# Optimization experiments

Measured on AMD Instinct MI355X. Metric: run time of the kernel, lower is better.

## Reference

```python
import jax, jax.numpy as jnp
import numpy as np

H = 128; NC = 100000; ND = 20000; NG = 50000; E = 150000; EP = 100000; L = 2

def _ln(x, g, b, eps=1e-5):
    mu = jnp.mean(x, -1, keepdims=True)
    v = jnp.mean((x - mu) ** 2, -1, keepdims=True)
    return (x - mu) * jax.lax.rsqrt(v + eps) * g + b

def _gelu(x):
    return jax.nn.gelu(x, approximate=False)  # torch nn.GELU default = exact erf

def _sage(x_src, x_dst, ei, Wl, bl, Wr):
    # PyG SAGEConv: mean-aggregate src features over incoming edges, lin_l(agg)+bias + lin_r(x_dst)
    n_dst = x_dst.shape[0]
    msg = x_src[ei[0]]                                   # [E, H] gather
    s = jax.ops.segment_sum(msg, ei[1], num_segments=n_dst)
    cnt = jax.ops.segment_sum(jnp.ones((ei.shape[1],), x_src.dtype), ei[1], num_segments=n_dst)
    agg = s / jnp.maximum(cnt, 1.0)[:, None]             # zero for isolated dst nodes
    return agg @ Wl + bl + x_dst @ Wr

def _make_ei(k, ns, nd, e):
    k1, k2 = jax.random.split(k)
    return jnp.stack([jax.random.randint(k1, (e,), 0, ns, dtype=jnp.int32),
                      jax.random.randint(k2, (e,), 0, nd, dtype=jnp.int32)])

def setup_inputs() -> dict:
    key = jax.random.key(0)
    ks = jax.random.split(key, 16)
    s = 0.05
    return {
        "x_chem": jax.random.normal(ks[0], (NC, 128), jnp.float32),
        "x_dis": jax.random.normal(ks[1], (ND, 128), jnp.float32),
        "gene_emb": jax.random.normal(ks[2], (NG, H), jnp.float32) * s,
        "proj_W": jax.random.normal(ks[3], (2, 128, H), jnp.float32) * s,
        "proj_b": jnp.zeros((2, H), jnp.float32),
        "proj_ln_g": jnp.ones((2, H), jnp.float32),
        "proj_ln_b": jnp.zeros((2, H), jnp.float32),
        "sage_Wl": jax.random.normal(ks[4], (L, 4, H, H), jnp.float32) * s,
        "sage_bl": jnp.zeros((L, 4, H), jnp.float32),
        "sage_Wr": jax.random.normal(ks[5], (L, 4, H, H), jnp.float32) * s,
        "ln_g": jnp.ones((L, 3, H), jnp.float32),
        "ln_b": jnp.zeros((L, 3, H), jnp.float32),
        "W_cd": jax.random.normal(ks[6], (H, H), jnp.float32) * s,
        "ei_c2d": _make_ei(ks[7], NC, ND, E),
        "ei_d2c": _make_ei(ks[8], ND, NC, E),
        "ei_c2g": _make_ei(ks[9], NC, NG, E),
        "ei_g2c": _make_ei(ks[10], NG, NC, E),
        "pos_edge": _make_ei(ks[11], NC, ND, EP),
        "neg_edge": _make_ei(ks[12], NC, ND, EP),
    }

def reference(x_chem, x_dis, gene_emb, proj_W, proj_b, proj_ln_g, proj_ln_b,
              sage_Wl, sage_bl, sage_Wr, ln_g, ln_b, W_cd,
              ei_c2d, ei_d2c, ei_c2g, ei_g2c, pos_edge, neg_edge):
    # init node states: Linear+LN+GELU for featured ntypes, embedding table for gene
    hc = _gelu(_ln(x_chem @ proj_W[0] + proj_b[0], proj_ln_g[0], proj_ln_b[0]))
    hd = _gelu(_ln(x_dis @ proj_W[1] + proj_b[1], proj_ln_g[1], proj_ln_b[1]))
    hg = gene_emb
    for l in range(L):
        # HeteroConv aggr='mean': chemical receives d2c (idx1) and g2c (idx3) -> mean of 2
        nc = 0.5 * (_sage(hd, hc, ei_d2c, sage_Wl[l, 1], sage_bl[l, 1], sage_Wr[l, 1])
                    + _sage(hg, hc, ei_g2c, sage_Wl[l, 3], sage_bl[l, 3], sage_Wr[l, 3]))
        nd = _sage(hc, hd, ei_c2d, sage_Wl[l, 0], sage_bl[l, 0], sage_Wr[l, 0])
        ng = _sage(hc, hg, ei_c2g, sage_Wl[l, 2], sage_bl[l, 2], sage_Wr[l, 2])
        # residual + LN + GELU (dropout is identity in eval mode)
        hc = _gelu(_ln(nc + hc, ln_g[l, 0], ln_b[l, 0]))
        hd = _gelu(_ln(nd + hd, ln_g[l, 1], ln_b[l, 1]))
        hg = _gelu(_ln(ng + hg, ln_g[l, 2], ln_b[l, 2]))
    def dec(ei):
        return ((hc[ei[0]] @ W_cd) * hd[ei[1]]).sum(-1)
    return dec(pos_edge), dec(neg_edge)
```

## Files before the change

kernel.cpp:

```cpp
#include <hip/hip_runtime.h>

#define HD 128

constexpr int T_NC = 100000;
constexpr int T_ND = 20000;
constexpr int T_NG = 50000;
constexpr int T_E  = 150000;
constexpr int T_EP = 100000;
constexpr int NMAT = 21;
constexpr int DEGN = 2 * T_NC + T_ND + T_NG;

typedef __attribute__((ext_vector_type(8))) short   s16x8;
typedef __attribute__((ext_vector_type(8))) __bf16  bf16x8;
typedef __attribute__((ext_vector_type(4))) float   f32x4;

union Frag { s16x8 s; bf16x8 b; };

__device__ __forceinline__ float gelu_f(float x) {
    return 0.5f * x * (1.0f + erff(x * 0.70710678118654752f));
}

__global__ void pack_weights(const float* __restrict__ proj_W,
                             const float* __restrict__ sage_Wl,
                             const float* __restrict__ sage_Wr,
                             const float* __restrict__ W_cd,
                             unsigned short* __restrict__ phi,
                             unsigned short* __restrict__ plo)
{
    int m = blockIdx.x;
    const float* W;
    const float* W2 = nullptr;
    bool transp = false;
    if (m < 2)        W = proj_W  + (size_t)m * HD * HD;
    else if (m < 10)  W = sage_Wl + (size_t)(m - 2) * HD * HD;
    else if (m < 18)  W = sage_Wr + (size_t)(m - 10) * HD * HD;
    else if (m == 18) { W = W_cd; transp = true; }
    else {
        int l = m - 19;
        W  = sage_Wr + (size_t)(l * 4 + 1) * HD * HD;
        W2 = sage_Wr + (size_t)(l * 4 + 3) * HD * HD;
    }

    int t = threadIdx.x;
    int kstep = t >> 6;
    int lane  = t & 63;
    int kbase = kstep * 32 + (lane >> 4) * 8;
    int c     = lane & 15;
    for (int cb = 0; cb < 8; ++cb) {
        int col = cb * 16 + c;
        size_t off = ((((size_t)m * 8 + cb) * 4 + kstep) * 64 + lane) * 8;
        #pragma unroll
        for (int j = 0; j < 8; ++j) {
            int k = kbase + j;
            float w = transp ? W[(size_t)col * HD + k] : W[(size_t)k * HD + col];
            if (W2) w += W2[(size_t)k * HD + col];
            __bf16 h = (__bf16)w;
            union { __bf16 b; unsigned short u; } ch, cl;
            ch.b = h;
            cl.b = (__bf16)(w - (float)h);
            phi[off + j] = ch.u;
            plo[off + j] = cl.u;
        }
    }
}

__global__ void conv_gene(const float* __restrict__ src, unsigned short* __restrict__ dst)
{
    size_t i = (size_t)(blockIdx.x * blockDim.x + threadIdx.x) * 8;
    if (i >= (size_t)T_NG * HD) return;
    f32x4 a0 = *(const f32x4*)(src + i);
    f32x4 a1 = *(const f32x4*)(src + i + 4);
    Frag u;
    u.b[0] = (__bf16)a0.x; u.b[1] = (__bf16)a0.y; u.b[2] = (__bf16)a0.z; u.b[3] = (__bf16)a0.w;
    u.b[4] = (__bf16)a1.x; u.b[5] = (__bf16)a1.y; u.b[6] = (__bf16)a1.z; u.b[7] = (__bf16)a1.w;
    *(s16x8*)(dst + i) = u.s;
}

__global__ void edge_count4(const int* __restrict__ eA, const int* __restrict__ eB,
                            const int* __restrict__ eC, const int* __restrict__ eD,
                            int gPer, int* __restrict__ deg)
{
    int seg = blockIdx.x / gPer;
    int e = (blockIdx.x % gPer) * 256 + threadIdx.x;
    if (e >= T_E) return;
    const int* ei = seg == 0 ? eA : seg == 1 ? eB : seg == 2 ? eC : eD;
    int off = seg == 0 ? 0 : seg == 1 ? T_NC : seg == 2 ? 2 * T_NC : 2 * T_NC + T_ND;
    atomicAdd(&deg[off + ei[T_E + e]], 1);
}

__global__ void scan_local(const int* __restrict__ deg, int* __restrict__ rp,
                           int* __restrict__ bsum, int N)
{
    __shared__ int wtot[4];
    int t = threadIdx.x;
    int lane = t & 63, w = t >> 6;
    int base = blockIdx.x * 1024 + t * 4;
    int v[4];
    #pragma unroll
    for (int j = 0; j < 4; ++j) v[j] = (base + j < N) ? deg[base + j] : 0;
    int p1 = v[0] + v[1];
    int p2 = p1 + v[2];
    int total = p2 + v[3];
    int sc = total;
    #pragma unroll
    for (int o = 1; o < 64; o <<= 1) {
        int y = __shfl_up(sc, o);
        if (lane >= o) sc += y;
    }
    if (lane == 63) wtot[w] = sc;
    __syncthreads();
    int woff = 0;
    for (int i = 0; i < w; ++i) woff += wtot[i];
    int ex = woff + sc - total;
    if (base + 0 < N) rp[base + 0] = ex;
    if (base + 1 < N) rp[base + 1] = ex + v[0];
    if (base + 2 < N) rp[base + 2] = ex + p1;
    if (base + 3 < N) rp[base + 3] = ex + p2;
    if (t == 255) bsum[blockIdx.x] = woff + sc;
}

__global__ void scan_tops(int* __restrict__ bsum, int B)
{
    int lane = threadIdx.x;
    int off = 0;
    for (int s = 0; s < B; s += 64) {
        int i = s + lane;
        int v = (i < B) ? bsum[i] : 0;
        int sc = v;
        #pragma unroll
        for (int o = 1; o < 64; o <<= 1) {
            int y = __shfl_up(sc, o);
            if (lane >= o) sc += y;
        }
        if (i < B) bsum[i] = off + sc - v;
        off += __shfl(sc, 63);
    }
}

__global__ void scan_add(int* __restrict__ rp, const int* __restrict__ bsum, int N)
{
    int base = blockIdx.x * 1024 + threadIdx.x * 4;
    int o = bsum[blockIdx.x];
    #pragma unroll
    for (int j = 0; j < 4; ++j)
        if (base + j < N) rp[base + j] += o;
}

__global__ void edge_fill4(const int* __restrict__ eA, const int* __restrict__ eB,
                           const int* __restrict__ eC, const int* __restrict__ eD,
                           int gPer, const int* __restrict__ rp,
                           int* __restrict__ fil, int* __restrict__ col)
{
    int seg = blockIdx.x / gPer;
    int e = (blockIdx.x % gPer) * 256 + threadIdx.x;
    if (e >= T_E) return;
    const int* ei = seg == 0 ? eA : seg == 1 ? eB : seg == 2 ? eC : eD;
    int off = seg == 0 ? 0 : seg == 1 ? T_NC : seg == 2 ? 2 * T_NC : 2 * T_NC + T_ND;
    int d = ei[T_E + e];
    int p = rp[off + d] + atomicAdd(&fil[off + d], 1);
    col[p] = ei[e];
}

struct Pair {
    const void* A;
    const int* rp; const int* dg; const int* col;
    int w; int fmt;
};
struct Seg {
    Pair p0, p1, p2;
    const float *bias0, *bias1, *g_ln, *b_ln;
    unsigned short* out;
    float scale;
    int np, use_res, M, nblk;
};

template<int MODE>
__global__ __launch_bounds__(256, 8)
void fused_gemm(Seg s0, Seg s1, Seg s2,
                const unsigned short* __restrict__ phi,
                const unsigned short* __restrict__ plo)
{
    __shared__ __align__(16) unsigned short As_hi[32 * HD];
    __shared__ __align__(16) unsigned short As_lo[32 * HD];
    __shared__ float psum[4][32];
    __shared__ float psq[4][32];

    int bid = blockIdx.x;
    Seg s;
    if (bid < s0.nblk) s = s0;
    else if (bid < s0.nblk + s1.nblk) { bid -= s0.nblk; s = s1; }
    else { bid -= s0.nblk + s1.nblk; s = s2; }

    const int tid  = threadIdx.x;
    const int w    = tid >> 6;
    const int lane = tid & 63;
    const int c    = lane & 15;
    const int hi4  = lane >> 4;
    const int row0 = bid * 32;

    f32x4 acc[2][2];
    #pragma unroll
    for (int rb = 0; rb < 2; ++rb)
        #pragma unroll
        for (int q = 0; q < 2; ++q) acc[rb][q] = (f32x4)0.f;

    for (int p = 0; p < s.np; ++p) {
        Pair P = (p == 0) ? s.p0 : (p == 1) ? s.p1 : s.p2;
        const bool gath = (P.rp != nullptr);

        __syncthreads();
        for (int it = 0; it < 2; ++it) {
            int u  = tid + it * 256;
            int r  = u >> 4;
            int k8 = (u & 15) * 8;
            int gr = row0 + r;
            Frag vh, vl;
            vh.s = (s16x8)0; vl.s = (s16x8)0;
            if (gr < s.M) {
                if (gath) {
                    float av[8] = {0.f, 0.f, 0.f, 0.f, 0.f, 0.f, 0.f, 0.f};
                    int st = P.rp[gr];
                    int d  = P.dg[gr];
                    const unsigned short* Ah = (const unsigned short*)P.A;
                    int i = 0;
                    for (; i + 2 <= d; i += 2) {
                        int e0 = P.col[st + i];
                        int e1 = P.col[st + i + 1];
                        Frag x0, x1;
                        x0.s = *(const s16x8*)(Ah + (size_t)e0 * HD + k8);
                        x1.s = *(const s16x8*)(Ah + (size_t)e1 * HD + k8);
                        #pragma unroll
                        for (int j = 0; j < 8; ++j)
                            av[j] += (float)x0.b[j] + (float)x1.b[j];
                    }
                    if (i < d) {
                        int e0 = P.col[st + i];
                        Frag x0;
                        x0.s = *(const s16x8*)(Ah + (size_t)e0 * HD + k8);
                        #pragma unroll
                        for (int j = 0; j < 8; ++j)
                            av[j] += (float)x0.b[j];
                    }
                    float rs = 1.f / (float)(d > 1 ? d : 1);
                    #pragma unroll
                    for (int j = 0; j < 8; ++j) {
                        float x = av[j] * rs;
                        __bf16 h = (__bf16)x;
                        vh.b[j] = h;
                        vl.b[j] = (__bf16)(x - (float)h);
                    }
                } else if (P.fmt) {
                    vh.s = *(const s16x8*)((const unsigned short*)P.A + (size_t)gr * HD + k8);
                } else {
                    const f32x4* ap = (const f32x4*)((const float*)P.A + (size_t)gr * HD + k8);
                    f32x4 a0 = ap[0], a1 = ap[1];
                    vh.b[0] = (__bf16)a0.x; vh.b[1] = (__bf16)a0.y;
                    vh.b[2] = (__bf16)a0.z; vh.b[3] = (__bf16)a0.w;
                    vh.b[4] = (__bf16)a1.x; vh.b[5] = (__bf16)a1.y;
                    vh.b[6] = (__bf16)a1.z; vh.b[7] = (__bf16)a1.w;
                }
            }
            int sidx = (r * HD + k8) ^ ((r & 7) << 3);
            *(s16x8*)(As_hi + sidx) = vh.s;
            if (gath) *(s16x8*)(As_lo + sidx) = vl.s;
        }
        __syncthreads();

        #pragma unroll
        for (int ks = 0; ks < 4; ++ks) {
            Frag bh[2], bl[2];
            #pragma unroll
            for (int q = 0; q < 2; ++q) {
                int cbG = w * 2 + q;
                size_t boff = ((((size_t)P.w * 8 + cbG) * 4 + ks) * 64 + lane) * 8;
                bh[q].s = *(const s16x8*)(phi + boff);
                bl[q].s = *(const s16x8*)(plo + boff);
            }
            #pragma unroll
            for (int rb = 0; rb < 2; ++rb) {
                int r = rb * 16 + c;
                int sidx = (r * HD + ks * 32 + hi4 * 8) ^ ((r & 7) << 3);
                Frag ah;
                ah.s = *(const s16x8*)(As_hi + sidx);
                #pragma unroll
                for (int q = 0; q < 2; ++q) {
                    acc[rb][q] = __builtin_amdgcn_mfma_f32_16x16x32_bf16(ah.b, bh[q].b, acc[rb][q], 0, 0, 0);
                    acc[rb][q] = __builtin_amdgcn_mfma_f32_16x16x32_bf16(ah.b, bl[q].b, acc[rb][q], 0, 0, 0);
                }
                if (gath) {
                    Frag al;
                    al.s = *(const s16x8*)(As_lo + sidx);
                    #pragma unroll
                    for (int q = 0; q < 2; ++q)
                        acc[rb][q] = __builtin_amdgcn_mfma_f32_16x16x32_bf16(al.b, bh[q].b, acc[rb][q], 0, 0, 0);
                }
            }
        }
    }

    if (MODE == 0) {
        __syncthreads();
        #pragma unroll
        for (int rb = 0; rb < 2; ++rb)
            #pragma unroll
            for (int q = 0; q < 2; ++q) {
                int col = (w * 2 + q) * 16 + c;
                #pragma unroll
                for (int reg = 0; reg < 4; ++reg) {
                    int row = rb * 16 + hi4 * 4 + reg;
                    union { __bf16 b; unsigned short u; } cv;
                    cv.b = (__bf16)acc[rb][q][reg];
                    As_hi[row * HD + col] = cv.u;
                }
            }
        __syncthreads();
        int row = tid >> 3;
        int c8  = (tid & 7) * 8;
        int gr  = row0 + row;
        if (gr < s.M) {
            *(s16x8*)(s.out + (size_t)gr * HD + c8)      = *(const s16x8*)(As_hi + row * HD + c8);
            *(s16x8*)(s.out + (size_t)gr * HD + 64 + c8) = *(const s16x8*)(As_hi + row * HD + 64 + c8);
        }
        return;
    }

    float bsum_[2], gl[2], bb[2];
    #pragma unroll
    for (int q = 0; q < 2; ++q) {
        int col = (w * 2 + q) * 16 + c;
        float b = 0.f;
        if (s.bias0) b += s.bias0[col];
        if (s.bias1) b += s.bias1[col];
        bsum_[q] = b;
        gl[q] = s.g_ln[col];
        bb[q] = s.b_ln[col];
    }

    float v[2][2][4];
    #pragma unroll
    for (int rb = 0; rb < 2; ++rb)
        #pragma unroll
        for (int q = 0; q < 2; ++q) {
            int col = (w * 2 + q) * 16 + c;
            #pragma unroll
            for (int reg = 0; reg < 4; ++reg) {
                int row = rb * 16 + hi4 * 4 + reg;
                float r_ = 0.f;
                if (s.use_res) {
                    int sx = (row * HD + col) ^ ((row & 7) << 3);
                    union { __bf16 b; unsigned short u; } cb; cb.u = As_hi[sx];
                    r_ = (float)cb.b;
                }
                v[rb][q][reg] = (acc[rb][q][reg] + bsum_[q]) * s.scale + r_;
            }
        }

    #pragma unroll
    for (int rb = 0; rb < 2; ++rb)
        #pragma unroll
        for (int reg = 0; reg < 4; ++reg) {
            float sm = v[rb][0][reg] + v[rb][1][reg];
            float qq = v[rb][0][reg] * v[rb][0][reg] + v[rb][1][reg] * v[rb][1][reg];
            #pragma unroll
            for (int m = 1; m <= 8; m <<= 1) {
                sm += __shfl_xor(sm, m);
                qq += __shfl_xor(qq, m);
            }
            if (c == 0) {
                int row = rb * 16 + hi4 * 4 + reg;
                psum[w][row] = sm;
                psq[w][row]  = qq;
            }
        }
    __syncthreads();

    #pragma unroll
    for (int rb = 0; rb < 2; ++rb)
        #pragma unroll
        for (int reg = 0; reg < 4; ++reg) {
            int row = rb * 16 + hi4 * 4 + reg;
            float S  = psum[0][row] + psum[1][row] + psum[2][row] + psum[3][row];
            float Q  = psq[0][row]  + psq[1][row]  + psq[2][row]  + psq[3][row];
            float mean = S * (1.f / 128.f);
            float var  = Q * (1.f / 128.f) - mean * mean;
            float rstd = rsqrtf(var + 1e-5f);
            #pragma unroll
            for (int q = 0; q < 2; ++q) {
                int col = (w * 2 + q) * 16 + c;
                float t = (v[rb][q][reg] - mean) * rstd * gl[q] + bb[q];
                union { __bf16 b; unsigned short u; } cv;
                cv.b = (__bf16)gelu_f(t);
                As_hi[row * HD + col] = cv.u;
            }
        }
    __syncthreads();

    {
        int row = tid >> 3;
        int c8  = (tid & 7) * 8;
        int gr  = row0 + row;
        if (gr < s.M) {
            *(s16x8*)(s.out + (size_t)gr * HD + c8)      = *(const s16x8*)(As_hi + row * HD + c8);
            *(s16x8*)(s.out + (size_t)gr * HD + 64 + c8) = *(const s16x8*)(As_hi + row * HD + 64 + c8);
        }
    }
}

__global__ void edge_score2(const int* __restrict__ pos, const int* __restrict__ neg,
                            const unsigned short* __restrict__ Hc,
                            const unsigned short* __restrict__ Qb,
                            float* __restrict__ out)
{
    int t = blockIdx.x * blockDim.x + threadIdx.x;
    int e = t >> 4;
    if (e >= 2 * T_EP) return;
    int lane = t & 15;
    const int* ei = pos;
    float* o = out;
    if (e >= T_EP) { e -= T_EP; ei = neg; o = out + T_EP; }
    int sI = ei[e];
    int dI = ei[T_EP + e];
    Frag p, h;
    p.s = *(const s16x8*)(Hc + (size_t)sI * HD + lane * 8);
    h.s = *(const s16x8*)(Qb + (size_t)dI * HD + lane * 8);
    float acc = 0.f;
    #pragma unroll
    for (int j = 0; j < 8; ++j)
        acc += (float)p.b[j] * (float)h.b[j];
    #pragma unroll
    for (int m = 1; m <= 8; m <<= 1) acc += __shfl_xor(acc, m);
    if (lane == 0) o[e] = acc;
}

extern "C" void kernel_launch(void* const* d_in, const int* in_sizes, int n_in,
                              void* d_out, int out_size, void* d_ws, size_t ws_size,
                              hipStream_t stream)
{
    const float* x_chem    = (const float*)d_in[0];
    const float* x_dis     = (const float*)d_in[1];
    const float* gene_emb  = (const float*)d_in[2];
    const float* proj_W    = (const float*)d_in[3];
    const float* proj_b    = (const float*)d_in[4];
    const float* proj_ln_g = (const float*)d_in[5];
    const float* proj_ln_b = (const float*)d_in[6];
    const float* sage_Wl   = (const float*)d_in[7];
    const float* sage_bl   = (const float*)d_in[8];
    const float* sage_Wr   = (const float*)d_in[9];
    const float* ln_g      = (const float*)d_in[10];
    const float* ln_b      = (const float*)d_in[11];
    const float* W_cd      = (const float*)d_in[12];
    const int*   ei_c2d    = (const int*)d_in[13];
    const int*   ei_d2c    = (const int*)d_in[14];
    const int*   ei_c2g    = (const int*)d_in[15];
    const int*   ei_g2c    = (const int*)d_in[16];
    const int*   pos_edge  = (const int*)d_in[17];
    const int*   neg_edge  = (const int*)d_in[18];
    float* out = (float*)d_out;

    unsigned short* us = (unsigned short*)d_ws;
    const size_t SC = (size_t)T_NC * HD, SD = (size_t)T_ND * HD, SG = (size_t)T_NG * HD;
    unsigned short* hc0  = us;
    unsigned short* hc1  = hc0 + SC;
    unsigned short* hd0  = hc1 + SC;
    unsigned short* hd1  = hd0 + SD;
    unsigned short* hgA  = hd1 + SD;
    unsigned short* hgB  = hgA + SG;
    unsigned short* geneB = hgB + SG;
    unsigned short* packHi = geneB + SG;
    unsigned short* packLo = packHi + (size_t)NMAT * HD * HD;
    int* ib  = (int*)(packLo + (size_t)NMAT * HD * HD);
    int* deg = ib;
    int* fil = deg + DEGN;
    int* rp  = fil + DEGN;
    int* col = rp + DEGN;
    int* bsum = col + 4 * T_E;
    unsigned short* Qb = hd1;

    const dim3 blk(256);
    const int gC = (T_NC + 31) / 32;
    const int gD = (T_ND + 31) / 32;
    const int gG = (T_NG + 31) / 32;
    const int gE256 = (T_E + 255) / 256;
    const int gScan = (DEGN + 1023) / 1024;
    const int gConv = (int)(((size_t)T_NG * HD / 8 + 255) / 256);
    const int OFF_DC = 0, OFF_GC = T_NC, OFF_CD = 2 * T_NC, OFF_CG = 2 * T_NC + T_ND;

    pack_weights<<<NMAT, blk, 0, stream>>>(proj_W, sage_Wl, sage_Wr, W_cd, packHi, packLo);
    conv_gene<<<gConv, blk, 0, stream>>>(gene_emb, geneB);
    hipMemsetAsync(deg, 0, (size_t)2 * DEGN * sizeof(int), stream);

    edge_count4<<<4 * gE256, blk, 0, stream>>>(ei_d2c, ei_g2c, ei_c2d, ei_c2g, gE256, deg);
    scan_local<<<gScan, blk, 0, stream>>>(deg, rp, bsum, DEGN);
    scan_tops<<<1, 64, 0, stream>>>(bsum, gScan);
    scan_add<<<gScan, blk, 0, stream>>>(rp, bsum, DEGN);
    edge_fill4<<<4 * gE256, blk, 0, stream>>>(ei_d2c, ei_g2c, ei_c2d, ei_c2g, gE256, rp, fil, col);

    Seg z{};

    {
        Seg pc{};
        pc.p0.A = x_chem; pc.p0.w = 0; pc.p0.fmt = 0;
        pc.np = 1; pc.use_res = 0;
        pc.bias0 = proj_b; pc.g_ln = proj_ln_g; pc.b_ln = proj_ln_b;
        pc.scale = 1.f; pc.out = hc0; pc.M = T_NC; pc.nblk = gC;
        Seg pd{};
        pd.p0.A = x_dis; pd.p0.w = 1; pd.p0.fmt = 0;
        pd.np = 1; pd.use_res = 0;
        pd.bias0 = proj_b + HD; pd.g_ln = proj_ln_g + HD; pd.b_ln = proj_ln_b + HD;
        pd.scale = 1.f; pd.out = hd0; pd.M = T_ND; pd.nblk = gD;
        fused_gemm<1><<<gC + gD, blk, 0, stream>>>(pc, pd, z, packHi, packLo);
    }

    for (int l = 0; l < 2; ++l) {
        const float* bl = sage_bl + (size_t)l * 4 * HD;
        const float* lg = ln_g + (size_t)l * 3 * HD;
        const float* lb = ln_b + (size_t)l * 3 * HD;
        const int wl = 2 + l * 4;
        const int wr = 10 + l * 4;
        const int wsum = 19 + l;

        const unsigned short* hcC = (l == 0) ? hc0 : hc1;
        unsigned short*       hcN = (l == 0) ? hc1 : hc0;
        const unsigned short* hdC = (l == 0) ? hd0 : hd1;
        unsigned short*       hdN = (l == 0) ? hd1 : hd0;
        const unsigned short* hgC = (l == 0) ? geneB : hgA;

        Seg sc{};
        sc.p0.A = hdC; sc.p0.fmt = 1; sc.p0.rp = rp + OFF_DC; sc.p0.dg = deg + OFF_DC; sc.p0.col = col; sc.p0.w = wl + 1;
        sc.p1.A = hgC; sc.p1.fmt = 1; sc.p1.rp = rp + OFF_GC; sc.p1.dg = deg + OFF_GC; sc.p1.col = col; sc.p1.w = wl + 3;
        sc.p2.A = hcC; sc.p2.fmt = 1; sc.p2.w = wsum;
        sc.np = 3; sc.use_res = 1;
        sc.bias0 = bl + 1 * HD; sc.bias1 = bl + 3 * HD;
        sc.scale = 0.5f; sc.g_ln = lg; sc.b_ln = lb;
        sc.out = hcN; sc.M = T_NC; sc.nblk = gC;

        Seg sd{};
        sd.p0.A = hcC; sd.p0.fmt = 1; sd.p0.rp = rp + OFF_CD; sd.p0.dg = deg + OFF_CD; sd.p0.col = col; sd.p0.w = wl + 0;
        sd.p1.A = hdC; sd.p1.fmt = 1; sd.p1.w = wr + 0;
        sd.np = 2; sd.use_res = 1;
        sd.bias0 = bl + 0 * HD;
        sd.scale = 1.f; sd.g_ln = lg + HD; sd.b_ln = lb + HD;
        sd.out = hdN; sd.M = T_ND; sd.nblk = gD;

        if (l == 0) {
            Seg sg{};
            sg.p0.A = hcC; sg.p0.fmt = 1; sg.p0.rp = rp + OFF_CG; sg.p0.dg = deg + OFF_CG; sg.p0.col = col; sg.p0.w = wl + 2;
            sg.p1.A = hgC; sg.p1.fmt = 1; sg.p1.w = wr + 2;
            sg.np = 2; sg.use_res = 1;
            sg.bias0 = bl + 2 * HD;
            sg.scale = 1.f; sg.g_ln = lg + 2 * HD; sg.b_ln = lb + 2 * HD;
            sg.out = hgA; sg.M = T_NG; sg.nblk = gG;
            fused_gemm<1><<<gC + gD + gG, blk, 0, stream>>>(sc, sd, sg, packHi, packLo);
        } else {
            fused_gemm<1><<<gC + gD, blk, 0, stream>>>(sc, sd, z, packHi, packLo);
        }
    }

    {
        Seg sq{};
        sq.p0.A = hd0; sq.p0.fmt = 1; sq.p0.w = 18;
        sq.np = 1; sq.use_res = 0;
        sq.scale = 1.f; sq.out = Qb; sq.M = T_ND; sq.nblk = gD;
        fused_gemm<0><<<gD, blk, 0, stream>>>(sq, z, z, packHi, packLo);
    }

    const int gEdge = (2 * T_EP * 16 + 255) / 256;
    edge_score2<<<gEdge, blk, 0, stream>>>(pos_edge, neg_edge, hc0, Qb, out);
}
```

Measured before the change: 362.3 us.

## Sort rows by degree within 32-row windows to balance gather work per wavefront

Adds a kernel that ranks nodes by in-degree inside each 32-row window and builds a permutation. The fused SAGE GEMM then reads and writes rows through this permutation, so lanes that gather neighbours together have similar degrees and wavefront divergence in the gather loop shrinks. Since ranking stays within a window, tile membership does not change, only the order of rows inside a tile. In exchange it adds a launch, an extra indirection load per row, and writes that are scattered within each tile.

```diff
diff --git a/kernel.cpp b/kernel.cpp
--- a/kernel.cpp
+++ b/kernel.cpp
@@ -9,6 +9,9 @@
 constexpr int T_EP = 100000;
 constexpr int NMAT = 21;
 constexpr int DEGN = 2 * T_NC + T_ND + T_NG;
+constexpr int WIN_C = (T_NC + 31) / 32;
+constexpr int WIN_D = (T_ND + 31) / 32;
+constexpr int WIN_G = (T_NG + 31) / 32;
 
 typedef __attribute__((ext_vector_type(8))) short   s16x8;
 typedef __attribute__((ext_vector_type(8))) __bf16  bf16x8;
@@ -161,6 +164,34 @@
     col[p] = ei[e];
 }
 
+__global__ void window_rank(const int* __restrict__ deg,
+                            int* __restrict__ perm_c, int* __restrict__ perm_d,
+                            int* __restrict__ perm_g)
+{
+    int gwin = (blockIdx.x * blockDim.x + threadIdx.x) >> 5;
+    int lane = threadIdx.x & 63;
+    int li = lane & 31;
+    if (gwin >= WIN_C + WIN_D + WIN_G) return;
+    int N, base; int* perm; int key = -1;
+    if (gwin < WIN_C)              { N = T_NC; base = gwin * 32;            perm = perm_c; }
+    else if (gwin < WIN_C + WIN_D) { N = T_ND; base = (gwin - WIN_C) * 32;  perm = perm_d; }
+    else                           { N = T_NG; base = (gwin - WIN_C - WIN_D) * 32; perm = perm_g; }
+    int i = base + li;
+    if (i < N) {
+        if (gwin < WIN_C)              key = deg[i] + deg[T_NC + i];
+        else if (gwin < WIN_C + WIN_D) key = deg[2 * T_NC + i];
+        else                           key = deg[2 * T_NC + T_ND + i];
+    }
+    int half = lane & 32;
+    int rank = 0;
+    #pragma unroll
+    for (int j = 0; j < 32; ++j) {
+        int kj = __shfl(key, half | j);
+        rank += (kj > key) || (kj == key && j < li);
+    }
+    if (i < N) perm[base + rank] = i;
+}
+
 struct Pair {
     const void* A;
     const int* rp; const int* dg; const int* col;
@@ -170,6 +201,7 @@
     Pair p0, p1, p2;
     const float *bias0, *bias1, *g_ln, *b_ln;
     unsigned short* out;
+    const int* perm;
     float scale;
     int np, use_res, M, nblk;
 };
@@ -213,10 +245,12 @@
             int u  = tid + it * 256;
             int r  = u >> 4;
             int k8 = (u & 15) * 8;
-            int gr = row0 + r;
+            int gr0 = row0 + r;
+            bool valid = gr0 < s.M;
+            int gr = (valid && s.perm) ? s.perm[gr0] : gr0;
             Frag vh, vl;
             vh.s = (s16x8)0; vl.s = (s16x8)0;
-            if (gr < s.M) {
+            if (valid) {
                 if (gath) {
                     float av[8] = {0.f, 0.f, 0.f, 0.f, 0.f, 0.f, 0.f, 0.f};
                     int st = P.rp[gr];
@@ -316,8 +350,9 @@
         __syncthreads();
         int row = tid >> 3;
         int c8  = (tid & 7) * 8;
-        int gr  = row0 + row;
-        if (gr < s.M) {
+        int gr0 = row0 + row;
+        if (gr0 < s.M) {
+            int gr = s.perm ? s.perm[gr0] : gr0;
             *(s16x8*)(s.out + (size_t)gr * HD + c8)      = *(const s16x8*)(As_hi + row * HD + c8);
             *(s16x8*)(s.out + (size_t)gr * HD + 64 + c8) = *(const s16x8*)(As_hi + row * HD + 64 + c8);
         }
@@ -398,8 +433,9 @@
     {
         int row = tid >> 3;
         int c8  = (tid & 7) * 8;
-        int gr  = row0 + row;
-        if (gr < s.M) {
+        int gr0 = row0 + row;
+        if (gr0 < s.M) {
+            int gr = s.perm ? s.perm[gr0] : gr0;
             *(s16x8*)(s.out + (size_t)gr * HD + c8)      = *(const s16x8*)(As_hi + row * HD + c8);
             *(s16x8*)(s.out + (size_t)gr * HD + 64 + c8) = *(const s16x8*)(As_hi + row * HD + 64 + c8);
         }
@@ -474,6 +510,9 @@
     int* rp  = fil + DEGN;
     int* col = rp + DEGN;
     int* bsum = col + 4 * T_E;
+    int* perm_c = bsum + 512;
+    int* perm_d = perm_c + T_NC;
+    int* perm_g = perm_d + T_ND;
     unsigned short* Qb = hd1;
 
     const dim3 blk(256);
@@ -483,6 +522,7 @@
     const int gE256 = (T_E + 255) / 256;
     const int gScan = (DEGN + 1023) / 1024;
     const int gConv = (int)(((size_t)T_NG * HD / 8 + 255) / 256);
+    const int gRank = ((WIN_C + WIN_D + WIN_G) * 32 + 255) / 256;
     const int OFF_DC = 0, OFF_GC = T_NC, OFF_CD = 2 * T_NC, OFF_CG = 2 * T_NC + T_ND;
 
     pack_weights<<<NMAT, blk, 0, stream>>>(proj_W, sage_Wl, sage_Wr, W_cd, packHi, packLo);
@@ -490,6 +530,7 @@
     hipMemsetAsync(deg, 0, (size_t)2 * DEGN * sizeof(int), stream);
 
     edge_count4<<<4 * gE256, blk, 0, stream>>>(ei_d2c, ei_g2c, ei_c2d, ei_c2g, gE256, deg);
+    window_rank<<<gRank, blk, 0, stream>>>(deg, perm_c, perm_d, perm_g);
     scan_local<<<gScan, blk, 0, stream>>>(deg, rp, bsum, DEGN);
     scan_tops<<<1, 64, 0, stream>>>(bsum, gScan);
     scan_add<<<gScan, blk, 0, stream>>>(rp, bsum, DEGN);
@@ -529,7 +570,7 @@
         sc.p0.A = hdC; sc.p0.fmt = 1; sc.p0.rp = rp + OFF_DC; sc.p0.dg = deg + OFF_DC; sc.p0.col = col; sc.p0.w = wl + 1;
         sc.p1.A = hgC; sc.p1.fmt = 1; sc.p1.rp = rp + OFF_GC; sc.p1.dg = deg + OFF_GC; sc.p1.col = col; sc.p1.w = wl + 3;
         sc.p2.A = hcC; sc.p2.fmt = 1; sc.p2.w = wsum;
-        sc.np = 3; sc.use_res = 1;
+        sc.np = 3; sc.use_res = 1; sc.perm = perm_c;
         sc.bias0 = bl + 1 * HD; sc.bias1 = bl + 3 * HD;
         sc.scale = 0.5f; sc.g_ln = lg; sc.b_ln = lb;
         sc.out = hcN; sc.M = T_NC; sc.nblk = gC;
@@ -537,7 +578,7 @@
         Seg sd{};
         sd.p0.A = hcC; sd.p0.fmt = 1; sd.p0.rp = rp + OFF_CD; sd.p0.dg = deg + OFF_CD; sd.p0.col = col; sd.p0.w = wl + 0;
         sd.p1.A = hdC; sd.p1.fmt = 1; sd.p1.w = wr + 0;
-        sd.np = 2; sd.use_res = 1;
+        sd.np = 2; sd.use_res = 1; sd.perm = perm_d;
         sd.bias0 = bl + 0 * HD;
         sd.scale = 1.f; sd.g_ln = lg + HD; sd.b_ln = lb + HD;
         sd.out = hdN; sd.M = T_ND; sd.nblk = gD;
@@ -546,7 +587,7 @@
             Seg sg{};
             sg.p0.A = hcC; sg.p0.fmt = 1; sg.p0.rp = rp + OFF_CG; sg.p0.dg = deg + OFF_CG; sg.p0.col = col; sg.p0.w = wl + 2;
             sg.p1.A = hgC; sg.p1.fmt = 1; sg.p1.w = wr + 2;
-            sg.np = 2; sg.use_res = 1;
+            sg.np = 2; sg.use_res = 1; sg.perm = perm_g;
             sg.bias0 = bl + 2 * HD;
             sg.scale = 1.f; sg.g_ln = lg + 2 * HD; sg.b_ln = lb + 2 * HD;
             sg.out = hgA; sg.M = T_NG; sg.nblk = gG;
```

New measurement: 382.4 us. +5.6%, slower.
